# Optimization experiments

Hardware: AMD Instinct MI355X
Metric: run time of the kernel (lower is better)

## Reference

```python
import jax, jax.numpy as jnp
import numpy as np

N_MOLS = 2048
ATOMS_PER_MOL = 32
BONDS_PER_MOL = 32  # undirected
N_ATOMS = N_MOLS * ATOMS_PER_MOL            # 65536
N_BONDS = 2 * N_MOLS * BONDS_PER_MOL        # 131072 directed
ATOM_FDIM = 133
BOND_RAW_FDIM = 14
BOND_FDIM = ATOM_FDIM + BOND_RAW_FDIM       # 147 (chemprop: f_atoms[src] ++ bond feats)
HIDDEN = 512
DEPTH = 3
CLS_HID = 512


def setup_inputs() -> dict:
    key = jax.random.key(0)
    ks = jax.random.split(key, 12)
    rng = np.random.default_rng(0)

    # --- graph structure: per-molecule random undirected bonds, both directions ---
    offs = (np.arange(N_MOLS) * ATOMS_PER_MOL)[:, None]
    u = (rng.integers(0, ATOMS_PER_MOL, (N_MOLS, BONDS_PER_MOL)) + offs).ravel()
    v = (rng.integers(0, ATOMS_PER_MOL, (N_MOLS, BONDS_PER_MOL)) + offs).ravel()
    bond_src = np.stack([u, v], axis=1).ravel().astype(np.int32)  # bond 2e: u->v, 2e+1: v->u
    bond_dst = np.stack([v, u], axis=1).ravel().astype(np.int32)
    b2revb = (np.arange(N_BONDS) ^ 1).astype(np.int32)
    atom_mol_id = np.repeat(np.arange(N_MOLS), ATOMS_PER_MOL).astype(np.int32)

    f_atoms = jax.random.normal(ks[0], (N_ATOMS, ATOM_FDIM), jnp.float32)
    bond_feat = jax.random.normal(ks[1], (N_BONDS, BOND_RAW_FDIM), jnp.float32)
    f_bonds = jnp.concatenate([f_atoms[jnp.asarray(bond_src)], bond_feat], axis=1)  # [B, 147]

    def lin(k, fan_in, fan_out):
        return jax.random.normal(k, (fan_in, fan_out), jnp.float32) / np.sqrt(fan_in)

    return {
        "f_atoms": f_atoms,
        "f_bonds": f_bonds,
        "W_i": lin(ks[2], BOND_FDIM, HIDDEN),
        "W_h": lin(ks[3], HIDDEN, HIDDEN),
        "W_o": lin(ks[4], ATOM_FDIM + HIDDEN, HIDDEN),
        "c1_W": lin(ks[5], HIDDEN, CLS_HID), "c1_b": jnp.zeros((CLS_HID,), jnp.float32),
        "c2_W": lin(ks[6], CLS_HID, CLS_HID), "c2_b": jnp.zeros((CLS_HID,), jnp.float32),
        "c3_W": lin(ks[7], CLS_HID, CLS_HID), "c3_b": jnp.zeros((CLS_HID,), jnp.float32),
        "out_W": lin(ks[8], CLS_HID, 1), "out_b": jnp.zeros((1,), jnp.float32),
        "bond_src": jnp.asarray(bond_src),
        "bond_dst": jnp.asarray(bond_dst),
        "b2revb": jnp.asarray(b2revb),
        "atom_mol_id": jnp.asarray(atom_mol_id),
    }


def reference(f_atoms, f_bonds, W_i, W_h, W_o,
              c1_W, c1_b, c2_W, c2_b, c3_W, c3_b, out_W, out_b,
              bond_src, bond_dst, b2revb, atom_mol_id):
    relu = jax.nn.relu
    seg = jax.ops.segment_sum

    inp = f_bonds @ W_i                      # [B, H]
    msg = relu(inp)
    for _ in range(DEPTH - 1):
        # sum of incoming bond messages at each atom (bond u->v is incoming to v)
        a_msg = seg(msg, bond_dst, num_segments=N_ATOMS)   # [A, H]
        msg = a_msg[bond_src] - msg[b2revb]                # exclude reverse bond
        msg = relu(inp + msg @ W_h)

    a_msg = seg(msg, bond_dst, num_segments=N_ATOMS)
    atom_h = relu(jnp.concatenate([f_atoms, a_msg], axis=1) @ W_o)  # [A, H]

    # mean aggregation per molecule
    mol_sum = seg(atom_h, atom_mol_id, num_segments=N_MOLS)
    counts = seg(jnp.ones((N_ATOMS,), atom_h.dtype), atom_mol_id, num_segments=N_MOLS)
    mol_vec = mol_sum / counts[:, None]      # [M, H]

    h = relu(mol_vec @ c1_W + c1_b)
    h = relu(h @ c2_W + c2_b)
    h = relu(h @ c3_W + c3_b)
    h = relu(h)  # extra ReLU in original Sequential (no-op after ReLU, kept for fidelity)
    logits = h @ out_W + out_b               # [M, 1]
    return logits
```

## Files before the change

kernel.cpp:

```cpp
#include <hip/hip_runtime.h>
#include <stdint.h>

typedef unsigned short u16;
typedef __attribute__((ext_vector_type(8))) short short8;
typedef __attribute__((ext_vector_type(4))) float f32x4;

static __device__ __forceinline__ float b2f(u16 u) {
    union { unsigned int i; float f; } x; x.i = ((unsigned int)u) << 16; return x.f;
}
static __device__ __forceinline__ u16 f2b(float f) {
    unsigned int x = __builtin_bit_cast(unsigned int, f);
    x += 0x7fffu + ((x >> 16) & 1u);
    return (u16)(x >> 16);
}
static __device__ __forceinline__ unsigned int cvt_pk(float lo, float hi) {
    unsigned int r;
    asm("v_cvt_pk_bf16_f32 %0, %1, %2" : "=v"(r) : "v"(lo), "v"(hi));
    return r;
}
static __device__ __forceinline__ void async16(const u16* g, u16* l) {
    __builtin_amdgcn_global_load_lds(
        (const __attribute__((address_space(1))) unsigned int*)g,
        (__attribute__((address_space(3))) unsigned int*)l, 16, 0, 0);
}

__global__ __launch_bounds__(512, 2) void gemm_ip_k(
    const u16* __restrict__ Abonds,
    const u16* __restrict__ Wc,
    const u16* __restrict__ amsg,
    u16* __restrict__ msg,
    const int* __restrict__ bsrc)
{
    __shared__ u16 lA[2][128 * 32];
    __shared__ u16 lB[2][512 * 32];
    const int t = threadIdx.x;
    const int r0 = blockIdx.x * 128;

    const int srow = t >> 2;
    const int ssl = (t & 3) ^ ((srow >> 1) & 3);
    const u16* agA = Abonds + (size_t)(r0 + srow) * 192 + ssl * 8;
    const u16* bgW = Wc + (size_t)srow * 704 + ssl * 8;
    const int e = r0 + srow;
    const u16* ar = amsg + (size_t)bsrc[e] * 512 + (t & 3) * 8;
    const u16* mr = msg + (size_t)(e ^ 1) * 512 + (t & 3) * 8;

    const int wid = t >> 6, lane = t & 63;
    const int wrow = (wid >> 2) * 64;
    const int wcol = (wid & 3) * 128;
    const int lrow = lane & 15, lk = lane >> 4;

    f32x4 acc[4][8] = {};
    short8 av, mv;

#define STAGE_B(k0, buf) { _Pragma("unroll") for (int i = 0; i < 4; ++i) \
        async16(bgW + (size_t)i * 90112 + (k0), &lB[buf][(i * 512 + t) * 8]); }
#define STAGE_A1(k0, buf) async16(agA + (k0), &lA[buf][t * 8]);
#define LOAD_A2(k0) { av = *(const short8*)(ar + ((k0) - 192)); \
                      mv = *(const short8*)(mr + ((k0) - 192)); }
#define WRITE_A2(buf) { union { short8 s; unsigned int u[4]; } o; \
        _Pragma("unroll") for (int p = 0; p < 4; ++p) \
            o.u[p] = cvt_pk(b2f((u16)av[2*p]) - b2f((u16)mv[2*p]), \
                            b2f((u16)av[2*p+1]) - b2f((u16)mv[2*p+1])); \
        *(short8*)&lA[buf][srow * 32 + ssl * 8] = o.s; }
#define COMPUTE(buf) { short8 af[4], bf[8]; \
        _Pragma("unroll") for (int m = 0; m < 4; ++m) { \
            int row = wrow + m * 16 + lrow; \
            af[m] = *(const short8*)&lA[buf][row * 32 + ((lk ^ ((row >> 1) & 3)) * 8)]; } \
        _Pragma("unroll") for (int n = 0; n < 8; ++n) { \
            int row = wcol + n * 16 + lrow; \
            bf[n] = *(const short8*)&lB[buf][row * 32 + ((lk ^ ((row >> 1) & 3)) * 8)]; } \
        _Pragma("unroll") for (int m = 0; m < 4; ++m) \
        _Pragma("unroll") for (int n = 0; n < 8; ++n) \
            acc[m][n] = __builtin_amdgcn_mfma_f32_16x16x32_bf16(af[m], bf[n], acc[m][n], 0, 0, 0); }

    STAGE_A1(0, 0)
    STAGE_B(0, 0)
    asm volatile("s_waitcnt vmcnt(0)" ::: "memory");
    __builtin_amdgcn_s_barrier();

#pragma unroll
    for (int s = 0; s < 22; ++s) {
        const int cur = s & 1;
        const int k1 = (s + 1) * 32;
        if (s < 21) {
            STAGE_B(k1, cur ^ 1)
            if (k1 < 192) {
                STAGE_A1(k1, cur ^ 1)
                asm volatile("s_waitcnt vmcnt(5)" ::: "memory");
            } else {
                LOAD_A2(k1)
                asm volatile("s_waitcnt vmcnt(6)" ::: "memory");
            }
        } else {
            asm volatile("s_waitcnt vmcnt(0)" ::: "memory");
        }
        __builtin_amdgcn_s_barrier();
        COMPUTE(cur)
        if (s < 21) {
            if (k1 >= 192) WRITE_A2(cur ^ 1)
            asm volatile("s_waitcnt lgkmcnt(0)" ::: "memory");
            __builtin_amdgcn_s_barrier();
        }
    }
#undef STAGE_B
#undef STAGE_A1
#undef LOAD_A2
#undef WRITE_A2
#undef COMPUTE

    const int rr0 = r0 + wrow + (lane >> 4) * 4;
    const int cc0 = wcol + (lane & 15);
#pragma unroll
    for (int m = 0; m < 4; ++m)
#pragma unroll
        for (int n = 0; n < 8; ++n)
#pragma unroll
            for (int r = 0; r < 4; ++r)
                msg[(size_t)(rr0 + m * 16 + r) * 512 + cc0 + n * 16] =
                    f2b(fmaxf(acc[m][n][r], 0.f));
}

__global__ __launch_bounds__(256, 2) void gemm_oop_k(
    const u16* __restrict__ A, const u16* __restrict__ Bt, u16* __restrict__ C,
    int M, int N, int K, int lda, int ldb, int nbn)
{
    __shared__ u16 lA[128 * 64];
    __shared__ u16 lB[128 * 64];
    const int tid = threadIdx.x;
    const int gid = blockIdx.x;
    const int q = (int)gridDim.x >> 3;
    const int gbi = (gid & 7) * q + (gid >> 3);
    const int mb = gbi / nbn, nb = gbi % nbn;

    const int wid = tid >> 6, lane = tid & 63;
    const int wr = (wid >> 1) * 64, wc = (wid & 1) * 64;
    const int lrow = lane & 15, lko = (lane >> 4) * 8;

    f32x4 acc[4][4] = {};
    const int srow = tid >> 3;
    const int scol = (tid & 7) * 8;
    const u16* ag = A + (size_t)(mb * 128 + srow) * lda + scol;
    const u16* bg = Bt + (size_t)(nb * 128 + srow) * ldb + scol;
    u16* la = &lA[tid * 8];
    u16* lb = &lB[tid * 8];

    for (int k0 = 0; k0 < K; k0 += 64) {
#pragma unroll
        for (int i = 0; i < 4; ++i) {
            async16(ag + (size_t)(i * 32) * lda + k0, la + i * 2048);
            async16(bg + (size_t)(i * 32) * ldb + k0, lb + i * 2048);
        }
        __syncthreads();
#pragma unroll
        for (int kk = 0; kk < 64; kk += 32) {
            short8 af[4], bf[4];
#pragma unroll
            for (int m = 0; m < 4; ++m)
                af[m] = *(const short8*)&lA[(wr + m * 16 + lrow) * 64 + kk + lko];
#pragma unroll
            for (int n = 0; n < 4; ++n)
                bf[n] = *(const short8*)&lB[(wc + n * 16 + lrow) * 64 + kk + lko];
#pragma unroll
            for (int m = 0; m < 4; ++m)
#pragma unroll
                for (int n = 0; n < 4; ++n)
                    acc[m][n] = __builtin_amdgcn_mfma_f32_16x16x32_bf16(af[m], bf[n], acc[m][n], 0, 0, 0);
        }
        __syncthreads();
    }

    const int r0 = mb * 128 + wr + (lane >> 4) * 4;
    const int c0 = nb * 128 + wc + (lane & 15);
#pragma unroll
    for (int m = 0; m < 4; ++m)
#pragma unroll
        for (int n = 0; n < 4; ++n)
#pragma unroll
            for (int r = 0; r < 4; ++r)
                C[(size_t)(r0 + m * 16 + r) * N + c0 + n * 16] = f2b(fmaxf(acc[m][n][r], 0.f));
}

template<bool FINAL>
__global__ __launch_bounds__(256) void segsum_k(
    const u16* __restrict__ msg, const int* __restrict__ bdst, u16* __restrict__ out)
{
    __shared__ float acc[32][256];
    const int m = blockIdx.x >> 1;
    const int t = threadIdx.x;
    const int c = (blockIdx.x & 1) * 256 + t;
#pragma unroll
    for (int a = 0; a < 32; ++a) acc[a][t] = 0.f;
    const int eb = m * 64;
    for (int ee = 0; ee < 64; ++ee) {
        int d = bdst[eb + ee] & 31;
        acc[d][t] += b2f(msg[(size_t)(eb + ee) * 512 + c]);
    }
#pragma unroll
    for (int a = 0; a < 32; ++a) {
        if constexpr (FINAL)
            out[(size_t)(m * 32 + a) * 704 + 160 + c] = f2b(acc[a][t]);
        else
            out[(size_t)(m * 32 + a) * 512 + c] = f2b(acc[a][t]);
    }
}

__global__ void cast_bonds_k(const float* __restrict__ fb, u16* __restrict__ Ab) {
    const int total = 131072 * 192;
    for (int idx = blockIdx.x * blockDim.x + threadIdx.x; idx < total; idx += gridDim.x * blockDim.x) {
        int b = idx / 192, cc = idx % 192;
        Ab[idx] = f2b((cc < 147) ? fb[(size_t)b * 147 + cc] : 0.f);
    }
}

__global__ void wcomb_k(const float* __restrict__ Wi, const float* __restrict__ Wh, u16* __restrict__ Wc) {
    const int total = 512 * 704;
    for (int idx = blockIdx.x * blockDim.x + threadIdx.x; idx < total; idx += gridDim.x * blockDim.x) {
        int n = idx / 704, k = idx % 704;
        float v = 0.f;
        if (k < 147) v = Wi[(size_t)k * 512 + n];
        else if (k >= 192) v = Wh[(size_t)(k - 192) * 512 + n];
        Wc[idx] = f2b(v);
    }
}

__global__ void wcat_k(const float* __restrict__ Wo, u16* __restrict__ Wt) {
    const int total = 512 * 704;
    for (int idx = blockIdx.x * blockDim.x + threadIdx.x; idx < total; idx += gridDim.x * blockDim.x) {
        int n = idx / 704, k = idx % 704;
        float v = 0.f;
        if (k < 133) v = Wo[(size_t)k * 512 + n];
        else if (k >= 160 && k < 672) v = Wo[(size_t)(k - 27) * 512 + n];
        Wt[idx] = f2b(v);
    }
}

__global__ void wtrans_k(const float* __restrict__ W, u16* __restrict__ Wt) {
    const int total = 512 * 512;
    for (int idx = blockIdx.x * blockDim.x + threadIdx.x; idx < total; idx += gridDim.x * blockDim.x) {
        int n = idx / 512, k = idx % 512;
        Wt[idx] = f2b(W[(size_t)k * 512 + n]);
    }
}

__global__ void cat_prep_k(const float* __restrict__ f_atoms, u16* __restrict__ Acat) {
    const int total = 65536 * 192;
    for (int idx = blockIdx.x * blockDim.x + threadIdx.x; idx < total; idx += gridDim.x * blockDim.x) {
        int a = idx / 192, j = idx % 192;
        int col = (j < 160) ? j : (512 + j);
        float v = (col < 133) ? f_atoms[(size_t)a * 133 + col] : 0.f;
        Acat[(size_t)a * 704 + col] = f2b(v);
    }
}

__global__ void mol_mean_k(const u16* __restrict__ ah, u16* __restrict__ mv) {
    const int m = blockIdx.x, t = threadIdx.x;
#pragma unroll
    for (int h = 0; h < 2; ++h) {
        int c = h * 256 + t;
        float s = 0.f;
        for (int a = 0; a < 32; ++a) s += b2f(ah[(size_t)(m * 32 + a) * 512 + c]);
        mv[(size_t)m * 512 + c] = f2b(s * 0.03125f);
    }
}

__global__ void logits_k(const u16* __restrict__ h, const float* __restrict__ ow,
                         const float* __restrict__ ob, float* __restrict__ out) {
    const int row = blockIdx.x * 4 + (threadIdx.x >> 6);
    const int lane = threadIdx.x & 63;
    const u16* hr = h + (size_t)row * 512 + lane * 8;
    float s = 0.f;
#pragma unroll
    for (int j = 0; j < 8; ++j) s += b2f(hr[j]) * ow[lane * 8 + j];
#pragma unroll
    for (int o = 32; o > 0; o >>= 1) s += __shfl_down(s, o);
    if (lane == 0) out[row] = s + ob[0];
}

extern "C" void kernel_launch(void* const* d_in, const int* in_sizes, int n_in,
                              void* d_out, int out_size, void* d_ws, size_t ws_size,
                              hipStream_t stream) {
    const float* f_atoms = (const float*)d_in[0];
    const float* f_bonds = (const float*)d_in[1];
    const float* W_i  = (const float*)d_in[2];
    const float* W_h  = (const float*)d_in[3];
    const float* W_o  = (const float*)d_in[4];
    const float* c1W  = (const float*)d_in[5];
    const float* c2W  = (const float*)d_in[7];
    const float* c3W  = (const float*)d_in[9];
    const float* outW = (const float*)d_in[11];
    const float* outB = (const float*)d_in[12];
    const int* bsrc = (const int*)d_in[13];
    const int* bdst = (const int*)d_in[14];
    float* out = (float*)d_out;
    (void)in_sizes; (void)n_in; (void)out_size;

    if (ws_size < 254672896u) return;

    char* w = (char*)d_ws;
    size_t off = 0;
    auto alloc = [&](size_t bytes) {
        size_t o = (off + 255) & ~(size_t)255; off = o + bytes; return (void*)(w + o);
    };

    u16* msg    = (u16*)alloc(134217728);
    u16* amsg   = (u16*)alloc(67108864);
    u16* Abonds = (u16*)alloc(50331648);
    u16* Wcomb  = (u16*)alloc(720896);
    u16* WcT    = (u16*)alloc(720896);
    u16* c1T    = (u16*)alloc(524288);
    u16* c2T    = (u16*)alloc(524288);
    u16* c3T    = (u16*)alloc(524288);
    u16* Acat  = amsg;
    u16* atomh = msg;
    u16* molv  = msg + 33554432;
    u16* h1    = molv + 1048576;
    u16* h2    = h1 + 1048576;
    u16* h3    = h2 + 1048576;

    cast_bonds_k<<<4096, 256, 0, stream>>>(f_bonds, Abonds);
    wcomb_k<<<512, 256, 0, stream>>>(W_i, W_h, Wcomb);
    wcat_k<<<512, 256, 0, stream>>>(W_o, WcT);
    wtrans_k<<<512, 256, 0, stream>>>(c1W, c1T);
    wtrans_k<<<512, 256, 0, stream>>>(c2W, c2T);
    wtrans_k<<<512, 256, 0, stream>>>(c3W, c3T);

    gemm_oop_k<<<4096, 256, 0, stream>>>(Abonds, Wcomb, msg, 131072, 512, 192, 192, 704, 4);

    for (int it = 0; it < 2; ++it) {
        segsum_k<false><<<4096, 256, 0, stream>>>(msg, bdst, amsg);
        gemm_ip_k<<<1024, 512, 0, stream>>>(Abonds, Wcomb, amsg, msg, bsrc);
    }

    cat_prep_k<<<4096, 256, 0, stream>>>(f_atoms, Acat);
    segsum_k<true><<<4096, 256, 0, stream>>>(msg, bdst, Acat);

    gemm_oop_k<<<2048, 256, 0, stream>>>(Acat, WcT, atomh, 65536, 512, 704, 704, 704, 4);
    mol_mean_k<<<2048, 256, 0, stream>>>(atomh, molv);

    gemm_oop_k<<<64, 256, 0, stream>>>(molv, c1T, h1, 2048, 512, 512, 512, 512, 4);
    gemm_oop_k<<<64, 256, 0, stream>>>(h1, c2T, h2, 2048, 512, 512, 512, 512, 4);
    gemm_oop_k<<<64, 256, 0, stream>>>(h2, c3T, h3, 2048, 512, 512, 512, 512, 4);
    logits_k<<<512, 256, 0, stream>>>(h3, outW, outB, out);
}
```

Baseline: 642.6 us.

## Add fused atom-output GEMM, restructure gemm_ip pipeline, vectorize segsum and mol_mean

The gemm_ip main loop moves to a single barrier per step with s_setprio raised around the MFMA block and reorders the B/A2 staging, aiming to cut barrier stalls. A new gemm_at_k replaces the concatenated 704-wide atom GEMM: it reads atom features and aggregated messages from separate buffers with a 128x512 tile and a K of 672, which removes cat_prep and the padded concat layout. segsum and mol_mean now process two bf16 columns per thread with packed loads and stores, and segsum uses one block per molecule. The single-barrier pipeline relies on the lgkmcnt wait plus the next iteration's barrier for LDS safety, which is a hazard risk.

```diff
diff --git a/kernel.cpp b/kernel.cpp
--- a/kernel.cpp
+++ b/kernel.cpp
@@ -75,38 +75,35 @@
 
     STAGE_A1(0, 0)
     STAGE_B(0, 0)
-    asm volatile("s_waitcnt vmcnt(0)" ::: "memory");
-    __builtin_amdgcn_s_barrier();
 
 #pragma unroll
     for (int s = 0; s < 22; ++s) {
         const int cur = s & 1;
         const int k1 = (s + 1) * 32;
+        __builtin_amdgcn_s_barrier();
         if (s < 21) {
-            STAGE_B(k1, cur ^ 1)
             if (k1 < 192) {
+                STAGE_B(k1, cur ^ 1)
                 STAGE_A1(k1, cur ^ 1)
                 asm volatile("s_waitcnt vmcnt(5)" ::: "memory");
             } else {
                 LOAD_A2(k1)
+                STAGE_B(k1, cur ^ 1)
                 asm volatile("s_waitcnt vmcnt(6)" ::: "memory");
             }
         } else {
             asm volatile("s_waitcnt vmcnt(0)" ::: "memory");
         }
-        __builtin_amdgcn_s_barrier();
+        __builtin_amdgcn_s_setprio(1);
         COMPUTE(cur)
-        if (s < 21) {
-            if (k1 >= 192) WRITE_A2(cur ^ 1)
-            asm volatile("s_waitcnt lgkmcnt(0)" ::: "memory");
-            __builtin_amdgcn_s_barrier();
-        }
+        __builtin_amdgcn_s_setprio(0);
+        if (s < 21 && k1 >= 192) WRITE_A2(cur ^ 1)
+        asm volatile("s_waitcnt lgkmcnt(0)" ::: "memory");
     }
 #undef STAGE_B
 #undef STAGE_A1
 #undef LOAD_A2
 #undef WRITE_A2
-#undef COMPUTE
 
     const int rr0 = r0 + wrow + (lane >> 4) * 4;
     const int cc0 = wcol + (lane & 15);
@@ -117,6 +114,80 @@
 #pragma unroll
             for (int r = 0; r < 4; ++r)
                 msg[(size_t)(rr0 + m * 16 + r) * 512 + cc0 + n * 16] =
+                    f2b(fmaxf(acc[m][n][r], 0.f));
+}
+
+__global__ __launch_bounds__(512, 2) void gemm_at_k(
+    const u16* __restrict__ Afeat,
+    const u16* __restrict__ WoT,
+    const u16* __restrict__ amsg,
+    u16* __restrict__ atomh)
+{
+    __shared__ u16 lA[2][128 * 32];
+    __shared__ u16 lB[2][512 * 32];
+    const int t = threadIdx.x;
+    const int a0 = blockIdx.x * 128;
+
+    const int srow = t >> 2;
+    const int ssl = (t & 3) ^ ((srow >> 1) & 3);
+    const u16* agF = Afeat + (size_t)(a0 + srow) * 160 + ssl * 8;
+    const u16* agM = amsg + (size_t)(a0 + srow) * 512 + ssl * 8;
+    const u16* bgW = WoT + (size_t)srow * 672 + ssl * 8;
+
+    const int wid = t >> 6, lane = t & 63;
+    const int wrow = (wid >> 2) * 64;
+    const int wcol = (wid & 3) * 128;
+    const int lrow = lane & 15, lk = lane >> 4;
+
+    f32x4 acc[4][8] = {};
+
+#define STAGE_B(k0, buf) { _Pragma("unroll") for (int i = 0; i < 4; ++i) \
+        async16(bgW + (size_t)i * 86016 + (k0), &lB[buf][(i * 512 + t) * 8]); }
+#define STAGE_AT(k0, buf) async16((k0) < 160 ? agF + (k0) : agM + ((k0) - 160), &lA[buf][t * 8]);
+#define COMPUTE(buf) { short8 af[4], bf[8]; \
+        _Pragma("unroll") for (int m = 0; m < 4; ++m) { \
+            int row = wrow + m * 16 + lrow; \
+            af[m] = *(const short8*)&lA[buf][row * 32 + ((lk ^ ((row >> 1) & 3)) * 8)]; } \
+        _Pragma("unroll") for (int n = 0; n < 8; ++n) { \
+            int row = wcol + n * 16 + lrow; \
+            bf[n] = *(const short8*)&lB[buf][row * 32 + ((lk ^ ((row >> 1) & 3)) * 8)]; } \
+        _Pragma("unroll") for (int m = 0; m < 4; ++m) \
+        _Pragma("unroll") for (int n = 0; n < 8; ++n) \
+            acc[m][n] = __builtin_amdgcn_mfma_f32_16x16x32_bf16(af[m], bf[n], acc[m][n], 0, 0, 0); }
+
+    STAGE_AT(0, 0)
+    STAGE_B(0, 0)
+
+#pragma unroll
+    for (int s = 0; s < 21; ++s) {
+        const int cur = s & 1;
+        const int k1 = (s + 1) * 32;
+        __builtin_amdgcn_s_barrier();
+        if (s < 20) {
+            STAGE_B(k1, cur ^ 1)
+            STAGE_AT(k1, cur ^ 1)
+            asm volatile("s_waitcnt vmcnt(5)" ::: "memory");
+        } else {
+            asm volatile("s_waitcnt vmcnt(0)" ::: "memory");
+        }
+        __builtin_amdgcn_s_setprio(1);
+        COMPUTE(cur)
+        __builtin_amdgcn_s_setprio(0);
+        asm volatile("s_waitcnt lgkmcnt(0)" ::: "memory");
+    }
+#undef STAGE_B
+#undef STAGE_AT
+#undef COMPUTE
+
+    const int rr0 = a0 + wrow + (lane >> 4) * 4;
+    const int cc0 = wcol + (lane & 15);
+#pragma unroll
+    for (int m = 0; m < 4; ++m)
+#pragma unroll
+        for (int n = 0; n < 8; ++n)
+#pragma unroll
+            for (int r = 0; r < 4; ++r)
+                atomh[(size_t)(rr0 + m * 16 + r) * 512 + cc0 + n * 16] =
                     f2b(fmaxf(acc[m][n][r], 0.f));
 }
 
@@ -180,28 +251,25 @@
                 C[(size_t)(r0 + m * 16 + r) * N + c0 + n * 16] = f2b(fmaxf(acc[m][n][r], 0.f));
 }
 
-template<bool FINAL>
 __global__ __launch_bounds__(256) void segsum_k(
     const u16* __restrict__ msg, const int* __restrict__ bdst, u16* __restrict__ out)
 {
-    __shared__ float acc[32][256];
-    const int m = blockIdx.x >> 1;
-    const int t = threadIdx.x;
-    const int c = (blockIdx.x & 1) * 256 + t;
-#pragma unroll
-    for (int a = 0; a < 32; ++a) acc[a][t] = 0.f;
+    __shared__ float acc[32][512];
+    const int m = blockIdx.x, t = threadIdx.x;
+    const int c = t * 2;
+#pragma unroll
+    for (int a = 0; a < 32; ++a) { acc[a][c] = 0.f; acc[a][c + 1] = 0.f; }
     const int eb = m * 64;
+#pragma unroll 4
     for (int ee = 0; ee < 64; ++ee) {
         int d = bdst[eb + ee] & 31;
-        acc[d][t] += b2f(msg[(size_t)(eb + ee) * 512 + c]);
-    }
-#pragma unroll
-    for (int a = 0; a < 32; ++a) {
-        if constexpr (FINAL)
-            out[(size_t)(m * 32 + a) * 704 + 160 + c] = f2b(acc[a][t]);
-        else
-            out[(size_t)(m * 32 + a) * 512 + c] = f2b(acc[a][t]);
-    }
+        unsigned int v = *(const unsigned int*)&msg[(size_t)(eb + ee) * 512 + c];
+        acc[d][c]     += b2f((u16)(v & 0xffffu));
+        acc[d][c + 1] += b2f((u16)(v >> 16));
+    }
+#pragma unroll
+    for (int a = 0; a < 32; ++a)
+        *(unsigned int*)&out[(size_t)(m * 32 + a) * 512 + c] = cvt_pk(acc[a][c], acc[a][c + 1]);
 }
 
 __global__ void cast_bonds_k(const float* __restrict__ fb, u16* __restrict__ Ab) {
@@ -209,6 +277,14 @@
     for (int idx = blockIdx.x * blockDim.x + threadIdx.x; idx < total; idx += gridDim.x * blockDim.x) {
         int b = idx / 192, cc = idx % 192;
         Ab[idx] = f2b((cc < 147) ? fb[(size_t)b * 147 + cc] : 0.f);
+    }
+}
+
+__global__ void cast_atoms_k(const float* __restrict__ fa, u16* __restrict__ Af) {
+    const int total = 65536 * 160;
+    for (int idx = blockIdx.x * blockDim.x + threadIdx.x; idx < total; idx += gridDim.x * blockDim.x) {
+        int a = idx / 160, j = idx % 160;
+        Af[idx] = f2b((j < 133) ? fa[(size_t)a * 133 + j] : 0.f);
     }
 }
 
@@ -223,13 +299,13 @@
     }
 }
 
-__global__ void wcat_k(const float* __restrict__ Wo, u16* __restrict__ Wt) {
-    const int total = 512 * 704;
+__global__ void wo672_k(const float* __restrict__ Wo, u16* __restrict__ Wt) {
+    const int total = 512 * 672;
     for (int idx = blockIdx.x * blockDim.x + threadIdx.x; idx < total; idx += gridDim.x * blockDim.x) {
-        int n = idx / 704, k = idx % 704;
+        int n = idx / 672, k = idx % 672;
         float v = 0.f;
         if (k < 133) v = Wo[(size_t)k * 512 + n];
-        else if (k >= 160 && k < 672) v = Wo[(size_t)(k - 27) * 512 + n];
+        else if (k >= 160) v = Wo[(size_t)(k - 27) * 512 + n];
         Wt[idx] = f2b(v);
     }
 }
@@ -242,25 +318,16 @@
     }
 }
 
-__global__ void cat_prep_k(const float* __restrict__ f_atoms, u16* __restrict__ Acat) {
-    const int total = 65536 * 192;
-    for (int idx = blockIdx.x * blockDim.x + threadIdx.x; idx < total; idx += gridDim.x * blockDim.x) {
-        int a = idx / 192, j = idx % 192;
-        int col = (j < 160) ? j : (512 + j);
-        float v = (col < 133) ? f_atoms[(size_t)a * 133 + col] : 0.f;
-        Acat[(size_t)a * 704 + col] = f2b(v);
-    }
-}
-
-__global__ void mol_mean_k(const u16* __restrict__ ah, u16* __restrict__ mv) {
-    const int m = blockIdx.x, t = threadIdx.x;
-#pragma unroll
-    for (int h = 0; h < 2; ++h) {
-        int c = h * 256 + t;
-        float s = 0.f;
-        for (int a = 0; a < 32; ++a) s += b2f(ah[(size_t)(m * 32 + a) * 512 + c]);
-        mv[(size_t)m * 512 + c] = f2b(s * 0.03125f);
-    }
+__global__ __launch_bounds__(256) void mol_mean_k(const u16* __restrict__ ah, u16* __restrict__ mv) {
+    const int m = blockIdx.x, t = threadIdx.x, c = t * 2;
+    float s0 = 0.f, s1 = 0.f;
+#pragma unroll 4
+    for (int a = 0; a < 32; ++a) {
+        unsigned int v = *(const unsigned int*)&ah[(size_t)(m * 32 + a) * 512 + c];
+        s0 += b2f((u16)(v & 0xffffu));
+        s1 += b2f((u16)(v >> 16));
+    }
+    *(unsigned int*)&mv[(size_t)m * 512 + c] = cvt_pk(s0 * 0.03125f, s1 * 0.03125f);
 }
 
 __global__ void logits_k(const u16* __restrict__ h, const float* __restrict__ ow,
@@ -306,11 +373,11 @@
     u16* amsg   = (u16*)alloc(67108864);
     u16* Abonds = (u16*)alloc(50331648);
     u16* Wcomb  = (u16*)alloc(720896);
-    u16* WcT    = (u16*)alloc(720896);
+    u16* WoT    = (u16*)alloc(720896);
     u16* c1T    = (u16*)alloc(524288);
     u16* c2T    = (u16*)alloc(524288);
     u16* c3T    = (u16*)alloc(524288);
-    u16* Acat  = amsg;
+    u16* Afeat = Abonds;
     u16* atomh = msg;
     u16* molv  = msg + 33554432;
     u16* h1    = molv + 1048576;
@@ -319,7 +386,7 @@
 
     cast_bonds_k<<<4096, 256, 0, stream>>>(f_bonds, Abonds);
     wcomb_k<<<512, 256, 0, stream>>>(W_i, W_h, Wcomb);
-    wcat_k<<<512, 256, 0, stream>>>(W_o, WcT);
+    wo672_k<<<512, 256, 0, stream>>>(W_o, WoT);
     wtrans_k<<<512, 256, 0, stream>>>(c1W, c1T);
     wtrans_k<<<512, 256, 0, stream>>>(c2W, c2T);
     wtrans_k<<<512, 256, 0, stream>>>(c3W, c3T);
@@ -327,14 +394,13 @@
     gemm_oop_k<<<4096, 256, 0, stream>>>(Abonds, Wcomb, msg, 131072, 512, 192, 192, 704, 4);
 
     for (int it = 0; it < 2; ++it) {
-        segsum_k<false><<<4096, 256, 0, stream>>>(msg, bdst, amsg);
+        segsum_k<<<2048, 256, 0, stream>>>(msg, bdst, amsg);
         gemm_ip_k<<<1024, 512, 0, stream>>>(Abonds, Wcomb, amsg, msg, bsrc);
     }
 
-    cat_prep_k<<<4096, 256, 0, stream>>>(f_atoms, Acat);
-    segsum_k<true><<<4096, 256, 0, stream>>>(msg, bdst, Acat);
-
-    gemm_oop_k<<<2048, 256, 0, stream>>>(Acat, WcT, atomh, 65536, 512, 704, 704, 704, 4);
+    segsum_k<<<2048, 256, 0, stream>>>(msg, bdst, amsg);
+    cast_atoms_k<<<2048, 256, 0, stream>>>(f_atoms, Afeat);
+    gemm_at_k<<<512, 512, 0, stream>>>(Afeat, WoT, amsg, atomh);
     mol_mean_k<<<2048, 256, 0, stream>>>(atomh, molv);
 
     gemm_oop_k<<<64, 256, 0, stream>>>(molv, c1T, h1, 2048, 512, 512, 512, 512, 4);
```

Result: slower. 657.9 us (+2.4%).
